# Kernel optimization log

Measured on AMD Instinct MI355X. Metric: run time of the kernel, lower is better.

## Reference

```python
import jax, jax.numpy as jnp
import numpy as np

EPS = 1e-8  # torch cosine_similarity eps


def setup_inputs() -> dict:
    key = jax.random.key(0)
    kx, kw = jax.random.split(key)
    B, D, C, K = 512, 512, 5994, 3
    x = jax.random.normal(kx, (B, D), dtype=jnp.float32)
    # xavier_normal over (D, C, K): std = sqrt(2 / (fan_in + fan_out))
    std = float(np.sqrt(2.0 / (D + C * K)))
    W = jax.random.normal(kw, (D, C, K), dtype=jnp.float32) * std
    return {"x": x, "W": W}


def reference(x, W):
    # cosine similarity along feature dim, without materializing [B, D, C, K]
    x_norm = jnp.maximum(jnp.linalg.norm(x, axis=1, keepdims=True), EPS)   # [B, 1]
    w_norm = jnp.maximum(jnp.linalg.norm(W, axis=0, keepdims=True), EPS)   # [1, C, K]
    xn = x / x_norm                                                        # [B, D]
    Wn = W / w_norm                                                        # [D, C, K]
    costh = jnp.einsum('bd,dck->bck', xn, Wn)                              # [B, C, K]
    return costh
```

## Files before the change

kernel.cpp:

```cpp
#include <hip/hip_runtime.h>
#include <hip/hip_bf16.h>
#include <stdint.h>


#define D_DIM 512
#define BM 128
#define BN 128
#define BK 64
#define KITERS (D_DIM / BK)
#define TILE_BYTES (64 * BM * 16)

typedef __bf16 bf16x8 __attribute__((ext_vector_type(8)));
typedef float f32x4 __attribute__((ext_vector_type(4)));

__device__ __forceinline__ unsigned short f2bf(float f) {
  union { float f; unsigned int u; } v; v.f = f;
  unsigned int u = v.u;
  u += 0x7fffu + ((u >> 16) & 1u);
  return (unsigned short)(u >> 16);
}

__device__ __forceinline__ void load_lds16(const void* g, void* l) {
  __builtin_amdgcn_global_load_lds(
      (__attribute__((address_space(1))) void*)(g),
      (__attribute__((address_space(3))) void*)(l), 16, 0, 0);
}

__global__ void prep_kernel(const float* __restrict__ x, const float* __restrict__ W,
                            unsigned short* __restrict__ An, unsigned short* __restrict__ Wt,
                            float* __restrict__ partial, int CK, int NT128, int nWtBlocks) {
  const int b = blockIdx.x;
  const int t = threadIdx.x;
  if (b < nWtBlocks) {
    __shared__ float red[8 * 128];
    const int ntile = b >> 3, gb = b & 7;
    const int cq = t & 31, dr = t >> 5;
    const int n0 = ntile * BN;
    const int nb = n0 + cq * 4;
    const int g = gb * 8 + dr;
    float ss0 = 0.f, ss1 = 0.f, ss2 = 0.f, ss3 = 0.f;
    unsigned int gr[4][4];
    if (n0 + BN <= CK) {
#pragma unroll
      for (int i = 0; i < 8; i += 2) {
        float4 v0 = *(const float4*)(W + (size_t)(g * 8 + i) * CK + nb);
        float4 v1 = *(const float4*)(W + (size_t)(g * 8 + i + 1) * CK + nb);
        ss0 += v0.x * v0.x + v1.x * v1.x; ss1 += v0.y * v0.y + v1.y * v1.y;
        ss2 += v0.z * v0.z + v1.z * v1.z; ss3 += v0.w * v0.w + v1.w * v1.w;
        gr[0][i >> 1] = (unsigned int)f2bf(v0.x) | ((unsigned int)f2bf(v1.x) << 16);
        gr[1][i >> 1] = (unsigned int)f2bf(v0.y) | ((unsigned int)f2bf(v1.y) << 16);
        gr[2][i >> 1] = (unsigned int)f2bf(v0.z) | ((unsigned int)f2bf(v1.z) << 16);
        gr[3][i >> 1] = (unsigned int)f2bf(v0.w) | ((unsigned int)f2bf(v1.w) << 16);
      }
    } else {
      float acc_ss[4] = {0.f, 0.f, 0.f, 0.f};
#pragma unroll
      for (int i = 0; i < 8; i += 2) {
#pragma unroll
        for (int e = 0; e < 4; ++e) {
          const int n = nb + e;
          const float f0 = (n < CK) ? W[(size_t)(g * 8 + i) * CK + n] : 0.f;
          const float f1 = (n < CK) ? W[(size_t)(g * 8 + i + 1) * CK + n] : 0.f;
          acc_ss[e] += f0 * f0 + f1 * f1;
          gr[e][i >> 1] = (unsigned int)f2bf(f0) | ((unsigned int)f2bf(f1) << 16);
        }
      }
      ss0 = acc_ss[0]; ss1 = acc_ss[1]; ss2 = acc_ss[2]; ss3 = acc_ss[3];
    }
    unsigned short* dst = Wt + (size_t)ntile * (TILE_BYTES / 2) + (size_t)g * (BM * 8) + (size_t)cq * 32;
#pragma unroll
    for (int e = 0; e < 4; ++e) {
      uint4 o; o.x = gr[e][0]; o.y = gr[e][1]; o.z = gr[e][2]; o.w = gr[e][3];
      *(uint4*)(dst + e * 8) = o;
    }
    *(float4*)(&red[dr * 128 + cq * 4]) = make_float4(ss0, ss1, ss2, ss3);
    __syncthreads();
    if (t < 128) {
      float s = 0.f;
#pragma unroll
      for (int k = 0; k < 8; ++k) s += red[k * 128 + t];
      partial[(size_t)gb * NT128 + n0 + t] = s;
    }
  } else {
    const int w = t >> 6, lane = t & 63;
    const int m = (b - nWtBlocks) * 4 + w;
    const float* xr = x + (size_t)m * D_DIM + lane * 8;
    float4 a = *(const float4*)(xr);
    float4 c = *(const float4*)(xr + 4);
    float s = a.x * a.x + a.y * a.y + a.z * a.z + a.w * a.w +
              c.x * c.x + c.y * c.y + c.z * c.z + c.w * c.w;
#pragma unroll
    for (int off = 32; off; off >>= 1) s += __shfl_xor(s, off, 64);
    const float inv = 1.f / fmaxf(sqrtf(s), 1e-8f);
    ushort4 o0, o1;
    o0.x = f2bf(a.x * inv); o0.y = f2bf(a.y * inv); o0.z = f2bf(a.z * inv); o0.w = f2bf(a.w * inv);
    o1.x = f2bf(c.x * inv); o1.y = f2bf(c.y * inv); o1.z = f2bf(c.z * inv); o1.w = f2bf(c.w * inv);
    const int mtile = m >> 7, r = m & 127;
    unsigned short* dst = An + (size_t)mtile * (TILE_BYTES / 2) + (size_t)lane * (BM * 8) + r * 8;
    *(ushort4*)dst = o0;
    *(ushort4*)(dst + 4) = o1;
  }
}

__global__ __launch_bounds__(256, 2) void gemm_kernel(const unsigned short* __restrict__ An,
                                                      const unsigned short* __restrict__ Wt,
                                                      const float* __restrict__ partial,
                                                      float* __restrict__ out, int CK, int NT128) {
  __shared__ __attribute__((aligned(16))) unsigned char lds[65536];
  const int total = gridDim.x;
  const int q = total >> 3, rr = total & 7;
  const int lin = blockIdx.x;
  const int xcd = lin & 7, idx = lin >> 3;
  const int wg = (xcd < rr) ? xcd * (q + 1) + idx : rr * (q + 1) + (xcd - rr) * q + idx;
  const int ntile = wg >> 2, mtile = wg & 3;

  const int t = threadIdx.x;
  const int lane = t & 63, w = t >> 6;
  const int wm = w >> 1, wn = w & 1;
  const int lrow = lane & 15;
  const int kg = lane >> 4;

  const unsigned char* srcA = (const unsigned char*)An + (size_t)mtile * TILE_BYTES;
  const unsigned char* srcB = (const unsigned char*)Wt + (size_t)ntile * TILE_BYTES;
  const int n0 = ntile * BN;

  f32x4 acc[4][4] = {};

#define STAGE(kt, sel)                                                        \
  {                                                                           \
    const size_t koff = (size_t)(kt) * 16384;                                 \
    unsigned char* bA = lds + (sel) * 32768;                                  \
    unsigned char* bB = bA + 16384;                                           \
    _Pragma("unroll")                                                         \
    for (int c = 0; c < 4; ++c) {                                             \
      const int off = w * 4096 + c * 1024;                                    \
      load_lds16(srcA + koff + off + lane * 16, bA + off);                    \
    }                                                                         \
    _Pragma("unroll")                                                         \
    for (int c = 0; c < 4; ++c) {                                             \
      const int off = w * 4096 + c * 1024;                                    \
      load_lds16(srcB + koff + off + lane * 16, bB + off);                    \
    }                                                                         \
  }

  STAGE(0, 0);
  __syncthreads();

  for (int kt = 0; kt < KITERS; ++kt) {
    const int cur = kt & 1;
    if (kt + 1 < KITERS) STAGE(kt + 1, cur ^ 1);

    const unsigned char* bA = lds + cur * 32768;
    const unsigned char* bB = bA + 16384;
    bf16x8 afrag[2][4], bfrag[2][4];
#pragma unroll
    for (int h = 0; h < 2; ++h)
#pragma unroll
      for (int i = 0; i < 4; ++i) {
        afrag[h][i] = *(const bf16x8*)(bA + (kg + 4 * h) * 2048 + (wm * 64 + i * 16 + lrow) * 16);
        bfrag[h][i] = *(const bf16x8*)(bB + (kg + 4 * h) * 2048 + (wn * 64 + i * 16 + lrow) * 16);
      }
#pragma unroll
    for (int i = 0; i < 4; ++i)
#pragma unroll
      for (int j = 0; j < 4; ++j) {
        acc[i][j] = __builtin_amdgcn_mfma_f32_16x16x32_bf16(afrag[0][i], bfrag[0][j], acc[i][j], 0, 0, 0);
        acc[i][j] = __builtin_amdgcn_mfma_f32_16x16x32_bf16(afrag[1][i], bfrag[1][j], acc[i][j], 0, 0, 0);
      }
    __syncthreads();
  }

  float* winv = (float*)lds;
  if (t < 128) {
    float s = 0.f;
#pragma unroll
    for (int k = 0; k < 8; ++k) s += partial[(size_t)k * NT128 + n0 + t];
    winv[t] = 1.f / fmaxf(sqrtf(s), 1e-8f);
  }
  __syncthreads();

#pragma unroll
  for (int j = 0; j < 4; ++j) {
    const int cl = wn * 64 + j * 16 + lrow;
    const int col = n0 + cl;
    if (col < CK) {
      const float wv = winv[cl];
#pragma unroll
      for (int i = 0; i < 4; ++i) {
#pragma unroll
        for (int jj = 0; jj < 4; ++jj) {
          const int row = mtile * BM + wm * 64 + i * 16 + kg * 4 + jj;
          out[(size_t)row * CK + col] = acc[i][j][jj] * wv;
        }
      }
    }
  }
}

extern "C" void kernel_launch(void* const* d_in, const int* in_sizes, int n_in,
                              void* d_out, int out_size, void* d_ws, size_t ws_size,
                              hipStream_t stream) {
  const float* x = (const float*)d_in[0];
  const float* W = (const float*)d_in[1];
  float* out = (float*)d_out;
  const int Bn = in_sizes[0] / D_DIM;
  const int CK = in_sizes[1] / D_DIM;
  const int ntiles = (CK + BN - 1) / BN;
  const int mtiles = Bn / BM;
  const int NT128 = ntiles * BN;

  unsigned char* ws = (unsigned char*)d_ws;
  float* partial = (float*)ws;
  unsigned short* An = (unsigned short*)(ws + 8 * (size_t)NT128 * 4);
  unsigned short* Wt = (unsigned short*)(ws + 8 * (size_t)NT128 * 4 + (size_t)mtiles * TILE_BYTES);

  const int nWtBlocks = ntiles * 8;
  const int nXBlocks = Bn / 4;
  hipLaunchKernelGGL(prep_kernel, dim3(nWtBlocks + nXBlocks), dim3(256), 0, stream,
                     x, W, An, Wt, partial, CK, NT128, nWtBlocks);
  hipLaunchKernelGGL(gemm_kernel, dim3(ntiles * mtiles), dim3(256), 0, stream,
                     An, Wt, partial, out, CK, NT128);
}
```

Before: 41.57 us.

## Triple-buffer K pipeline with finer K steps and LDS-staged coalesced output stores

Splits the K loop into 16 steps of 32 and uses a three-slot LDS ring, so each step needs only one barrier, guarded by explicit vmcnt waits on the async global-to-LDS loads. LDS use drops to 48KB and launch bounds rise to 3 blocks per CU for more occupancy. For full tiles, the epilogue stages the scaled accumulators per wave in LDS and writes them as row-contiguous float4 stores instead of scattered scalar stores. The cost is more barrier and loop overhead per unit of K, and float4 stores that may be unaligned because the row stride CK is not a multiple of 4.

```diff
diff --git a/kernel.cpp b/kernel.cpp
--- a/kernel.cpp
+++ b/kernel.cpp
@@ -6,8 +6,7 @@
 #define D_DIM 512
 #define BM 128
 #define BN 128
-#define BK 64
-#define KITERS (D_DIM / BK)
+#define KITERS 16
 #define TILE_BYTES (64 * BM * 16)
 
 typedef __bf16 bf16x8 __attribute__((ext_vector_type(8)));
@@ -102,16 +101,16 @@
   }
 }
 
-__global__ __launch_bounds__(256, 2) void gemm_kernel(const unsigned short* __restrict__ An,
+__global__ __launch_bounds__(256, 3) void gemm_kernel(const unsigned short* __restrict__ An,
                                                       const unsigned short* __restrict__ Wt,
                                                       const float* __restrict__ partial,
                                                       float* __restrict__ out, int CK, int NT128) {
-  __shared__ __attribute__((aligned(16))) unsigned char lds[65536];
+  __shared__ __attribute__((aligned(16))) unsigned char lds[49152];
   const int total = gridDim.x;
   const int q = total >> 3, rr = total & 7;
   const int lin = blockIdx.x;
   const int xcd = lin & 7, idx = lin >> 3;
-  const int wg = (xcd < rr) ? xcd * (q + 1) + idx : rr * (q + 1) + (xcd - rr) * q + idx;
+  const int wg = ((xcd < rr) ? xcd * (q + 1) : rr * (q + 1) + (xcd - rr) * q) + idx;
   const int ntile = wg >> 2, mtile = wg & 3;
 
   const int t = threadIdx.x;
@@ -123,53 +122,57 @@
   const unsigned char* srcA = (const unsigned char*)An + (size_t)mtile * TILE_BYTES;
   const unsigned char* srcB = (const unsigned char*)Wt + (size_t)ntile * TILE_BYTES;
   const int n0 = ntile * BN;
+  const bool full = (n0 + BN <= CK);
 
   f32x4 acc[4][4] = {};
 
 #define STAGE(kt, sel)                                                        \
   {                                                                           \
-    const size_t koff = (size_t)(kt) * 16384;                                 \
-    unsigned char* bA = lds + (sel) * 32768;                                  \
-    unsigned char* bB = bA + 16384;                                           \
+    const size_t koff = (size_t)(kt) * 8192;                                  \
+    unsigned char* bAw = lds + (sel) * 16384;                                 \
+    unsigned char* bBw = bAw + 8192;                                          \
     _Pragma("unroll")                                                         \
-    for (int c = 0; c < 4; ++c) {                                             \
-      const int off = w * 4096 + c * 1024;                                    \
-      load_lds16(srcA + koff + off + lane * 16, bA + off);                    \
+    for (int c = 0; c < 2; ++c) {                                             \
+      const int off = c * 4096 + t * 16;                                      \
+      load_lds16(srcA + koff + off, bAw + off);                               \
     }                                                                         \
     _Pragma("unroll")                                                         \
-    for (int c = 0; c < 4; ++c) {                                             \
-      const int off = w * 4096 + c * 1024;                                    \
-      load_lds16(srcB + koff + off + lane * 16, bB + off);                    \
+    for (int c = 0; c < 2; ++c) {                                             \
+      const int off = c * 4096 + t * 16;                                      \
+      load_lds16(srcB + koff + off, bBw + off);                               \
     }                                                                         \
   }
 
   STAGE(0, 0);
+
+#pragma unroll
+  for (int kt = 0; kt < KITERS; ++kt) {
+    if (kt + 1 < KITERS) STAGE(kt + 1, (kt + 1) % 3);
+    __builtin_amdgcn_sched_barrier(0);
+    if (kt + 1 < KITERS) {
+      asm volatile("s_waitcnt vmcnt(4)" ::: "memory");
+    } else {
+      asm volatile("s_waitcnt vmcnt(0)" ::: "memory");
+    }
+    __builtin_amdgcn_s_barrier();
+    __builtin_amdgcn_sched_barrier(0);
+
+    const unsigned char* bA = lds + (kt % 3) * 16384;
+    const unsigned char* bB = bA + 8192;
+    bf16x8 afrag[4], bfrag[4];
+#pragma unroll
+    for (int i = 0; i < 4; ++i) {
+      afrag[i] = *(const bf16x8*)(bA + kg * 2048 + (wm * 64 + i * 16 + lrow) * 16);
+      bfrag[i] = *(const bf16x8*)(bB + kg * 2048 + (wn * 64 + i * 16 + lrow) * 16);
+    }
+#pragma unroll
+    for (int i = 0; i < 4; ++i)
+#pragma unroll
+      for (int j = 0; j < 4; ++j)
+        acc[i][j] = __builtin_amdgcn_mfma_f32_16x16x32_bf16(afrag[i], bfrag[j], acc[i][j], 0, 0, 0);
+  }
+
   __syncthreads();
-
-  for (int kt = 0; kt < KITERS; ++kt) {
-    const int cur = kt & 1;
-    if (kt + 1 < KITERS) STAGE(kt + 1, cur ^ 1);
-
-    const unsigned char* bA = lds + cur * 32768;
-    const unsigned char* bB = bA + 16384;
-    bf16x8 afrag[2][4], bfrag[2][4];
-#pragma unroll
-    for (int h = 0; h < 2; ++h)
-#pragma unroll
-      for (int i = 0; i < 4; ++i) {
-        afrag[h][i] = *(const bf16x8*)(bA + (kg + 4 * h) * 2048 + (wm * 64 + i * 16 + lrow) * 16);
-        bfrag[h][i] = *(const bf16x8*)(bB + (kg + 4 * h) * 2048 + (wn * 64 + i * 16 + lrow) * 16);
-      }
-#pragma unroll
-    for (int i = 0; i < 4; ++i)
-#pragma unroll
-      for (int j = 0; j < 4; ++j) {
-        acc[i][j] = __builtin_amdgcn_mfma_f32_16x16x32_bf16(afrag[0][i], bfrag[0][j], acc[i][j], 0, 0, 0);
-        acc[i][j] = __builtin_amdgcn_mfma_f32_16x16x32_bf16(afrag[1][i], bfrag[1][j], acc[i][j], 0, 0, 0);
-      }
-    __syncthreads();
-  }
-
   float* winv = (float*)lds;
   if (t < 128) {
     float s = 0.f;
@@ -178,20 +181,42 @@
     winv[t] = 1.f / fmaxf(sqrtf(s), 1e-8f);
   }
   __syncthreads();
-
-#pragma unroll
-  for (int j = 0; j < 4; ++j) {
-    const int cl = wn * 64 + j * 16 + lrow;
-    const int col = n0 + cl;
-    if (col < CK) {
-      const float wv = winv[cl];
-#pragma unroll
-      for (int i = 0; i < 4; ++i) {
-#pragma unroll
-        for (int jj = 0; jj < 4; ++jj) {
-          const int row = mtile * BM + wm * 64 + i * 16 + kg * 4 + jj;
-          out[(size_t)row * CK + col] = acc[i][j][jj] * wv;
-        }
+  float wv[4];
+#pragma unroll
+  for (int j = 0; j < 4; ++j) wv[j] = winv[wn * 64 + j * 16 + lrow];
+
+  if (full) {
+    float* stg = (float*)(lds + 1024) + w * 2176;
+    const int l15 = lane & 15, l4 = lane >> 4;
+#pragma unroll
+    for (int half = 0; half < 2; ++half) {
+#pragma unroll
+      for (int di = 0; di < 2; ++di)
+#pragma unroll
+        for (int j = 0; j < 4; ++j)
+#pragma unroll
+          for (int jj = 0; jj < 4; ++jj)
+            stg[(di * 16 + kg * 4 + jj) * 68 + j * 16 + lrow] = acc[half * 2 + di][j][jj] * wv[j];
+#pragma unroll
+      for (int s = 0; s < 8; ++s) {
+        const int rl = s * 4 + l4;
+        float4 v = *(float4*)&stg[rl * 68 + l15 * 4];
+        const int row = mtile * BM + wm * 64 + half * 32 + rl;
+        *(float4*)&out[(size_t)row * CK + n0 + wn * 64 + l15 * 4] = v;
+      }
+    }
+  } else {
+#pragma unroll
+    for (int j = 0; j < 4; ++j) {
+      const int col = n0 + wn * 64 + j * 16 + lrow;
+      if (col < CK) {
+#pragma unroll
+        for (int i = 0; i < 4; ++i)
+#pragma unroll
+          for (int jj = 0; jj < 4; ++jj) {
+            const int row = mtile * BM + wm * 64 + i * 16 + kg * 4 + jj;
+            out[(size_t)row * CK + col] = acc[i][j][jj] * wv[j];
+          }
       }
     }
   }
```

Measured after the change: 35.88 us. 1.16x faster.
